# Kernel optimization log

Hardware: AMD Instinct MI355X
Metric: run time of the kernel (lower is better)

## Reference

```python
import jax, jax.numpy as jnp
import numpy as np

E, B, S, H = 8, 16, 512, 1024
LN_EPS = 1e-12


def setup_inputs() -> dict:
    key = jax.random.key(0)
    k = jax.random.split(key, 5)
    return {
        "hidden_states": jax.random.normal(k[0], (B, S, H), dtype=jnp.float32),
        "input_tensor": jax.random.normal(k[1], (B, S, H), dtype=jnp.float32),
        "expert_idx": jax.random.randint(k[2], (B,), 0, E, dtype=jnp.int64)
        if jax.config.jax_enable_x64 else jax.random.randint(k[2], (B,), 0, E, dtype=jnp.int32),
        "W": jax.random.normal(k[3], (E, H, H), dtype=jnp.float32) * (1.0 / np.sqrt(H)),
        "b": jax.random.normal(k[4], (E, H), dtype=jnp.float32) * 0.02,
        "gamma": jnp.ones((H,), dtype=jnp.float32),
        "beta": jnp.zeros((H,), dtype=jnp.float32),
    }


def reference(hidden_states, input_tensor, expert_idx, W, b, gamma, beta):
    # All-expert dense forward, matching single_select_fwd's stacked compute.
    # all_out: [E, B, S, H]
    all_out = jnp.einsum("bsh,ehd->ebsd", hidden_states, W) + b[:, None, None, :]
    # slice_for_expert: pick (expert_idx[b], b) for each batch row -> [B, S, H]
    selected = all_out[expert_idx, jnp.arange(hidden_states.shape[0])]
    # dropout is identity in eval mode; residual + LayerNorm
    x = selected + input_tensor
    mu = jnp.mean(x, axis=-1, keepdims=True)
    var = jnp.mean(jnp.square(x - mu), axis=-1, keepdims=True)
    return (x - mu) * jax.lax.rsqrt(var + LN_EPS) * gamma + beta
```

## Files before the change

kernel.cpp:

```cpp
#include <hip/hip_runtime.h>
#include <hip/hip_bf16.h>

#define BB 16
#define SS 512
#define HH 1024

typedef __attribute__((ext_vector_type(4))) float f32x4;
typedef __attribute__((ext_vector_type(8))) short bhalf8;

static __device__ __forceinline__ unsigned int pack2(float a, float b) {
    __hip_bfloat162 h = __float22bfloat162_rn(make_float2(a, b));
    union { __hip_bfloat162 h; unsigned int u; } cv;
    cv.h = h;
    return cv.u;
}

static __device__ __forceinline__ unsigned short bf16u(float f) {
    union { float f; unsigned int u; } c; c.f = f;
    unsigned int r = c.u + 0x7FFFu + ((c.u >> 16) & 1u);
    return (unsigned short)(r >> 16);
}

static __device__ __forceinline__ float ubf16(unsigned short u) {
    union { unsigned int u; float f; } c; c.u = ((unsigned int)u) << 16;
    return c.f;
}

__global__ __launch_bounds__(256)
void prep_kernel(const float* __restrict__ W, const float* __restrict__ hid,
                 const int* __restrict__ eidx, unsigned short* __restrict__ Wt,
                 unsigned short* __restrict__ hidb)
{
    int bid = blockIdx.x;
    int t = threadIdx.x;
    if (bid < 2048) {
        __shared__ float lds[32 * 132];
        int e  = bid >> 8;
        bool used = false;
        for (int b = 0; b < BB; ++b) used = used || (eidx[b] == e);
        if (!used) return;
        int rem = bid & 255;
        int kt = rem >> 3, dt = rem & 7;
#pragma unroll
        for (int i = 0; i < 4; ++i) {
            int idx = t + i * 256;
            int row = idx >> 5, col4 = idx & 31;
            float4 v = *(const float4*)(W + ((size_t)e << 20)
                        + (size_t)(kt * 32 + row) * HH + dt * 128 + col4 * 4);
            float* dst = &lds[row * 132 + col4 * 4];
            dst[0] = v.x; dst[1] = v.y; dst[2] = v.z; dst[3] = v.w;
        }
        __syncthreads();
        int d = t >> 1, kh = t & 1;
        unsigned int u[8];
#pragma unroll
        for (int p = 0; p < 8; ++p) {
            float a = lds[(kh * 16 + p * 2)     * 132 + d];
            float b = lds[(kh * 16 + p * 2 + 1) * 132 + d];
            u[p] = pack2(a, b);
        }
        unsigned short* dst = Wt + ((size_t)e << 20)
                            + (size_t)(dt * 128 + d) * HH + kt * 32 + kh * 16;
        *reinterpret_cast<uint4*>(dst)     = make_uint4(u[0], u[1], u[2], u[3]);
        *reinterpret_cast<uint4*>(dst + 8) = make_uint4(u[4], u[5], u[6], u[7]);
    } else {
        int bid2 = bid - 2048;
        int r = bid2 * 2 + (t >> 7);
        int col = (t & 127) * 8;
        const float* src = hid + (size_t)r * HH + col;
        float4 v0 = *(const float4*)(src);
        float4 v1 = *(const float4*)(src + 4);
        uint4 o;
        o.x = pack2(v0.x, v0.y); o.y = pack2(v0.z, v0.w);
        o.z = pack2(v1.x, v1.y); o.w = pack2(v1.z, v1.w);
        *reinterpret_cast<uint4*>(hidb + (size_t)r * HH + col) = o;
    }
}

__global__ __launch_bounds__(512, 4)
void gemm8_kernel(const unsigned short* __restrict__ hidb,
                  const int* __restrict__ eidx,
                  const unsigned short* __restrict__ Wt,
                  unsigned short* __restrict__ ybuf)
{
    __shared__ char ldsA[4 * 8192];
    __shared__ char ldsW[4 * 8192];

    int bx  = blockIdx.x;
    int swz = (bx & 7) * 64 + (bx >> 3);
    int bt   = swz >> 5;
    int tile = swz & 31;
    int mt = tile >> 3, nt = tile & 7;
    int e = eidx[bt];

    int t = threadIdx.x, wave = t >> 6, lane = t & 63;
    int l15 = lane & 15, g = lane >> 4;
    int wm = wave >> 1, wn = wave & 1;

    int brow = bt * SS + mt * 128;
    int ncol0 = nt * 128;

    const unsigned short* asrc;
    const unsigned short* wsrc;
    int coff;
    {
        int c = t;
        int line = c >> 3, p = c & 7, q = p ^ (line & 7);
        int row = line * 2 + (q >> 2), s = q & 3;
        asrc = hidb + (size_t)(brow + row) * HH + s * 8;
        wsrc = Wt + ((size_t)e << 20) + (size_t)(ncol0 + row) * HH + s * 8;
        coff = c * 16;
    }

    auto stage = [&](int ks, int b) {
        __builtin_amdgcn_global_load_lds(
            (const __attribute__((address_space(1))) void*)(asrc + ks * 32),
            (__attribute__((address_space(3))) void*)(ldsA + b * 8192 + coff),
            16, 0, 0);
        __builtin_amdgcn_global_load_lds(
            (const __attribute__((address_space(1))) void*)(wsrc + ks * 32),
            (__attribute__((address_space(3))) void*)(ldsW + b * 8192 + coff),
            16, 0, 0);
    };

    f32x4 acc[2][4] = {};

    auto body = [&](int ks, bool do_stage) {
        const char* Af = ldsA + (ks & 3) * 8192;
        const char* Wf = ldsW + (ks & 3) * 8192;
        bhalf8 af[2], bf[4];
#pragma unroll
        for (int mf = 0; mf < 2; ++mf) {
            int r = wm * 32 + mf * 16 + l15;
            int line = r >> 1;
            int p = (g + ((r & 1) << 2)) ^ (line & 7);
            af[mf] = *reinterpret_cast<const bhalf8*>(Af + line * 128 + p * 16);
        }
#pragma unroll
        for (int nf = 0; nf < 4; ++nf) {
            int d = wn * 64 + nf * 16 + l15;
            int line = d >> 1;
            int p = (g + ((d & 1) << 2)) ^ (line & 7);
            bf[nf] = *reinterpret_cast<const bhalf8*>(Wf + line * 128 + p * 16);
        }
        if (do_stage) stage(ks + 3, (ks + 3) & 3);
        __builtin_amdgcn_s_barrier();
        __builtin_amdgcn_s_setprio(1);
#pragma unroll
        for (int mf = 0; mf < 2; ++mf)
#pragma unroll
            for (int nf = 0; nf < 4; ++nf)
                acc[mf][nf] = __builtin_amdgcn_mfma_f32_16x16x32_bf16(
                    af[mf], bf[nf], acc[mf][nf], 0, 0, 0);
        __builtin_amdgcn_s_setprio(0);
    };

    stage(0, 0); stage(1, 1); stage(2, 2);
    asm volatile("s_waitcnt vmcnt(4)" ::: "memory");
    __builtin_amdgcn_s_barrier();

    for (int ks = 0; ks < 29; ++ks) {
        body(ks, true);
        asm volatile("s_waitcnt vmcnt(4)" ::: "memory");
        __builtin_amdgcn_s_barrier();
    }
    body(29, false);
    asm volatile("s_waitcnt vmcnt(2)" ::: "memory");
    __builtin_amdgcn_s_barrier();
    body(30, false);
    asm volatile("s_waitcnt vmcnt(0)" ::: "memory");
    __builtin_amdgcn_s_barrier();
    body(31, false);

#pragma unroll
    for (int nf = 0; nf < 4; ++nf) {
        int dcol = ncol0 + wn * 64 + nf * 16 + l15;
#pragma unroll
        for (int mf = 0; mf < 2; ++mf)
#pragma unroll
            for (int j = 0; j < 4; ++j) {
                int srow = brow + wm * 32 + mf * 16 + g * 4 + j;
                ybuf[(size_t)srow * HH + dcol] = bf16u(acc[mf][nf][j]);
            }
    }
}

__global__ __launch_bounds__(256)
void post_kernel(const unsigned short* __restrict__ ybuf,
                 const float* __restrict__ inp,
                 const int* __restrict__ eidx, const float* __restrict__ bias,
                 const float* __restrict__ gamma, const float* __restrict__ beta,
                 float* __restrict__ out)
{
    int bid = blockIdx.x;
    int row = ((bid & 7) << 10) | (bid >> 3);
    int bt = row >> 9;
    int e = eidx[bt];
    int t = threadIdx.x;

    size_t base = (size_t)row * HH + t * 4;
    ushort4 yv = *reinterpret_cast<const ushort4*>(&ybuf[base]);
    float4 iv = *reinterpret_cast<const float4*>(&inp[base]);
    float4 bv = *reinterpret_cast<const float4*>(&bias[e * HH + t * 4]);
    float4 x;
    x.x = ubf16(yv.x) + iv.x + bv.x;
    x.y = ubf16(yv.y) + iv.y + bv.y;
    x.z = ubf16(yv.z) + iv.z + bv.z;
    x.w = ubf16(yv.w) + iv.w + bv.w;

    float s1 = x.x + x.y + x.z + x.w;
    float s2 = x.x * x.x + x.y * x.y + x.z * x.z + x.w * x.w;
#pragma unroll
    for (int off = 32; off > 0; off >>= 1) {
        s1 += __shfl_xor(s1, off, 64);
        s2 += __shfl_xor(s2, off, 64);
    }
    __shared__ float red[8];
    if ((t & 63) == 0) { red[(t >> 6) * 2] = s1; red[(t >> 6) * 2 + 1] = s2; }
    __syncthreads();
    float S1 = red[0] + red[2] + red[4] + red[6];
    float S2 = red[1] + red[3] + red[5] + red[7];
    float mu  = S1 * (1.0f / HH);
    float var = S2 * (1.0f / HH) - mu * mu;
    float rs = rsqrtf(var + 1e-12f);

    float4 gv = *reinterpret_cast<const float4*>(&gamma[t * 4]);
    float4 be = *reinterpret_cast<const float4*>(&beta[t * 4]);
    float4 o;
    o.x = (x.x - mu) * rs * gv.x + be.x;
    o.y = (x.y - mu) * rs * gv.y + be.y;
    o.z = (x.z - mu) * rs * gv.z + be.z;
    o.w = (x.w - mu) * rs * gv.w + be.w;
    *reinterpret_cast<float4*>(&out[base]) = o;
}

extern "C" void kernel_launch(void* const* d_in, const int* in_sizes, int n_in,
                              void* d_out, int out_size, void* d_ws, size_t ws_size,
                              hipStream_t stream) {
    const float* hid   = (const float*)d_in[0];
    const float* inp   = (const float*)d_in[1];
    const int*   eidx  = (const int*)d_in[2];
    const float* W     = (const float*)d_in[3];
    const float* bias  = (const float*)d_in[4];
    const float* gamma = (const float*)d_in[5];
    const float* beta  = (const float*)d_in[6];
    float* out = (float*)d_out;

    unsigned short* Wt   = (unsigned short*)d_ws;
    unsigned short* hidb = (unsigned short*)((char*)d_ws + (16u << 20));
    unsigned short* ybuf = (unsigned short*)((char*)d_ws + (32u << 20));

    prep_kernel<<<6144, 256, 0, stream>>>(W, hid, eidx, Wt, hidb);
    gemm8_kernel<<<512, 512, 0, stream>>>(hidb, eidx, Wt, ybuf);
    post_kernel<<<BB * SS, 256, 0, stream>>>(ybuf, inp, eidx, bias, gamma, beta, out);
}
```

Baseline: 56.24 us.

## Load W fragments directly from global into registers using k-tiled layout

The prep kernel now writes the transposed bf16 weights in a k-tile-major layout (32-wide k slabs, contiguous per tile). The GEMM kernel drops the LDS staging buffer for W and instead has each lane load its MFMA B fragments straight from global memory into registers, double-buffered one k-step ahead, with adjusted vmcnt waits. This halves LDS usage and removes LDS traffic for W, which may raise occupancy. The cost is uncoalesced-ish per-lane global loads and the W reuse across the two wm waves going through cache instead of LDS.

```diff
diff --git a/kernel.cpp b/kernel.cpp
--- a/kernel.cpp
+++ b/kernel.cpp
@@ -28,7 +28,7 @@
 
 __global__ __launch_bounds__(256)
 void prep_kernel(const float* __restrict__ W, const float* __restrict__ hid,
-                 const int* __restrict__ eidx, unsigned short* __restrict__ Wt,
+                 const int* __restrict__ eidx, unsigned short* __restrict__ Wt2,
                  unsigned short* __restrict__ hidb)
 {
     int bid = blockIdx.x;
@@ -59,8 +59,8 @@
             float b = lds[(kh * 16 + p * 2 + 1) * 132 + d];
             u[p] = pack2(a, b);
         }
-        unsigned short* dst = Wt + ((size_t)e << 20)
-                            + (size_t)(dt * 128 + d) * HH + kt * 32 + kh * 16;
+        unsigned short* dst = Wt2 + ((size_t)e << 20)
+                            + (size_t)kt * 32768 + (size_t)(dt * 128 + d) * 32 + kh * 16;
         *reinterpret_cast<uint4*>(dst)     = make_uint4(u[0], u[1], u[2], u[3]);
         *reinterpret_cast<uint4*>(dst + 8) = make_uint4(u[4], u[5], u[6], u[7]);
     } else {
@@ -80,11 +80,10 @@
 __global__ __launch_bounds__(512, 4)
 void gemm8_kernel(const unsigned short* __restrict__ hidb,
                   const int* __restrict__ eidx,
-                  const unsigned short* __restrict__ Wt,
+                  const unsigned short* __restrict__ Wt2,
                   unsigned short* __restrict__ ybuf)
 {
     __shared__ char ldsA[4 * 8192];
-    __shared__ char ldsW[4 * 8192];
 
     int bx  = blockIdx.x;
     int swz = (bx & 7) * 64 + (bx >> 3);
@@ -101,34 +100,43 @@
     int ncol0 = nt * 128;
 
     const unsigned short* asrc;
-    const unsigned short* wsrc;
     int coff;
     {
         int c = t;
         int line = c >> 3, p = c & 7, q = p ^ (line & 7);
         int row = line * 2 + (q >> 2), s = q & 3;
         asrc = hidb + (size_t)(brow + row) * HH + s * 8;
-        wsrc = Wt + ((size_t)e << 20) + (size_t)(ncol0 + row) * HH + s * 8;
         coff = c * 16;
     }
 
-    auto stage = [&](int ks, int b) {
+    auto stageA = [&](int ks, int b) {
         __builtin_amdgcn_global_load_lds(
             (const __attribute__((address_space(1))) void*)(asrc + ks * 32),
             (__attribute__((address_space(3))) void*)(ldsA + b * 8192 + coff),
             16, 0, 0);
-        __builtin_amdgcn_global_load_lds(
-            (const __attribute__((address_space(1))) void*)(wsrc + ks * 32),
-            (__attribute__((address_space(3))) void*)(ldsW + b * 8192 + coff),
-            16, 0, 0);
     };
 
+    const unsigned short* wlane = Wt2 + ((size_t)e << 20)
+                                + (size_t)(ncol0 + wn * 64 + l15) * 32 + g * 8;
+
+    bhalf8 bf[4], bfp[4];
+    auto loadW = [&](int ks, bhalf8* dst) {
+        const unsigned short* p = wlane + (size_t)ks * 32768;
+#pragma unroll
+        for (int nf = 0; nf < 4; ++nf)
+            dst[nf] = *reinterpret_cast<const bhalf8*>(p + nf * 512);
+    };
+
     f32x4 acc[2][4] = {};
 
-    auto body = [&](int ks, bool do_stage) {
+    stageA(0, 0); stageA(1, 1); stageA(2, 2);
+    loadW(0, bf);
+    asm volatile("s_waitcnt vmcnt(6)" ::: "memory");
+    __builtin_amdgcn_s_barrier();
+
+    for (int ks = 0; ks < 32; ++ks) {
         const char* Af = ldsA + (ks & 3) * 8192;
-        const char* Wf = ldsW + (ks & 3) * 8192;
-        bhalf8 af[2], bf[4];
+        bhalf8 af[2];
 #pragma unroll
         for (int mf = 0; mf < 2; ++mf) {
             int r = wm * 32 + mf * 16 + l15;
@@ -136,14 +144,8 @@
             int p = (g + ((r & 1) << 2)) ^ (line & 7);
             af[mf] = *reinterpret_cast<const bhalf8*>(Af + line * 128 + p * 16);
         }
-#pragma unroll
-        for (int nf = 0; nf < 4; ++nf) {
-            int d = wn * 64 + nf * 16 + l15;
-            int line = d >> 1;
-            int p = (g + ((d & 1) << 2)) ^ (line & 7);
-            bf[nf] = *reinterpret_cast<const bhalf8*>(Wf + line * 128 + p * 16);
-        }
-        if (do_stage) stage(ks + 3, (ks + 3) & 3);
+        if (ks <= 30) loadW(ks + 1, bfp);
+        if (ks <= 28) stageA(ks + 3, (ks + 3) & 3);
         __builtin_amdgcn_s_barrier();
         __builtin_amdgcn_s_setprio(1);
 #pragma unroll
@@ -153,24 +155,13 @@
                 acc[mf][nf] = __builtin_amdgcn_mfma_f32_16x16x32_bf16(
                     af[mf], bf[nf], acc[mf][nf], 0, 0, 0);
         __builtin_amdgcn_s_setprio(0);
-    };
-
-    stage(0, 0); stage(1, 1); stage(2, 2);
-    asm volatile("s_waitcnt vmcnt(4)" ::: "memory");
-    __builtin_amdgcn_s_barrier();
-
-    for (int ks = 0; ks < 29; ++ks) {
-        body(ks, true);
-        asm volatile("s_waitcnt vmcnt(4)" ::: "memory");
+#pragma unroll
+        for (int nf = 0; nf < 4; ++nf) bf[nf] = bfp[nf];
+        if (ks < 29)       { asm volatile("s_waitcnt vmcnt(6)" ::: "memory"); }
+        else if (ks == 29) { asm volatile("s_waitcnt vmcnt(5)" ::: "memory"); }
+        else if (ks == 30) { asm volatile("s_waitcnt vmcnt(4)" ::: "memory"); }
         __builtin_amdgcn_s_barrier();
     }
-    body(29, false);
-    asm volatile("s_waitcnt vmcnt(2)" ::: "memory");
-    __builtin_amdgcn_s_barrier();
-    body(30, false);
-    asm volatile("s_waitcnt vmcnt(0)" ::: "memory");
-    __builtin_amdgcn_s_barrier();
-    body(31, false);
 
 #pragma unroll
     for (int nf = 0; nf < 4; ++nf) {
@@ -246,11 +237,11 @@
     const float* beta  = (const float*)d_in[6];
     float* out = (float*)d_out;
 
-    unsigned short* Wt   = (unsigned short*)d_ws;
+    unsigned short* Wt2  = (unsigned short*)d_ws;
     unsigned short* hidb = (unsigned short*)((char*)d_ws + (16u << 20));
     unsigned short* ybuf = (unsigned short*)((char*)d_ws + (32u << 20));
 
-    prep_kernel<<<6144, 256, 0, stream>>>(W, hid, eidx, Wt, hidb);
-    gemm8_kernel<<<512, 512, 0, stream>>>(hidb, eidx, Wt, ybuf);
+    prep_kernel<<<6144, 256, 0, stream>>>(W, hid, eidx, Wt2, hidb);
+    gemm8_kernel<<<512, 512, 0, stream>>>(hidb, eidx, Wt2, ybuf);
     post_kernel<<<BB * SS, 256, 0, stream>>>(ybuf, inp, eidx, bias, gamma, beta, out);
 }
```

New measurement: 70.92 us. +26.1%, slower.

## Shrink GEMM tile to 128x64 with 4 waves and double buffering

Applied to the files above, without the earlier changes.

Changes the expert GEMM from 128x128 tiles run by 512 threads with a 4-stage LDS ring to 128x64 tiles run by 256 threads with a 2-stage double buffer, launching 1024 blocks instead of 512. Each wave now computes a 64x32 sub-tile, and the hand-tuned vmcnt/barrier schedule is replaced by a __syncthreads at the end of each k-step. The intent is to raise occupancy and block count with a smaller LDS footprint. The cost is shallower prefetch depth, a full memory wait every iteration, and less operand reuse per tile, since the hidden-state tile is now loaded twice as often.

```diff
diff --git a/kernel.cpp b/kernel.cpp
--- a/kernel.cpp
+++ b/kernel.cpp
@@ -77,20 +77,20 @@
     }
 }
 
-__global__ __launch_bounds__(512, 4)
+__global__ __launch_bounds__(256, 5)
 void gemm8_kernel(const unsigned short* __restrict__ hidb,
                   const int* __restrict__ eidx,
                   const unsigned short* __restrict__ Wt,
                   unsigned short* __restrict__ ybuf)
 {
-    __shared__ char ldsA[4 * 8192];
-    __shared__ char ldsW[4 * 8192];
+    __shared__ char ldsA[2 * 8192];
+    __shared__ char ldsW[2 * 4096];
 
     int bx  = blockIdx.x;
-    int swz = (bx & 7) * 64 + (bx >> 3);
-    int bt   = swz >> 5;
-    int tile = swz & 31;
-    int mt = tile >> 3, nt = tile & 7;
+    int swz = (bx & 7) * 128 + (bx >> 3);
+    int bt   = swz >> 6;
+    int rem  = swz & 63;
+    int mt = rem >> 4, nt = rem & 15;
     int e = eidx[bt];
 
     int t = threadIdx.x, wave = t >> 6, lane = t & 63;
@@ -98,88 +98,86 @@
     int wm = wave >> 1, wn = wave & 1;
 
     int brow = bt * SS + mt * 128;
-    int ncol0 = nt * 128;
-
-    const unsigned short* asrc;
+    int ncol0 = nt * 64;
+
+    const unsigned short* asrc[2];
+    int aoff[2];
+#pragma unroll
+    for (int i = 0; i < 2; ++i) {
+        int c = t + i * 256;
+        int line = c >> 3, p = c & 7, q = p ^ (line & 7);
+        int row = line * 2 + (q >> 2), s = q & 3;
+        asrc[i] = hidb + (size_t)(brow + row) * HH + s * 8;
+        aoff[i] = c * 16;
+    }
     const unsigned short* wsrc;
-    int coff;
+    int woff;
     {
         int c = t;
         int line = c >> 3, p = c & 7, q = p ^ (line & 7);
         int row = line * 2 + (q >> 2), s = q & 3;
-        asrc = hidb + (size_t)(brow + row) * HH + s * 8;
         wsrc = Wt + ((size_t)e << 20) + (size_t)(ncol0 + row) * HH + s * 8;
-        coff = c * 16;
-    }
-
-    auto stage = [&](int ks, int b) {
-        __builtin_amdgcn_global_load_lds(
-            (const __attribute__((address_space(1))) void*)(asrc + ks * 32),
-            (__attribute__((address_space(3))) void*)(ldsA + b * 8192 + coff),
-            16, 0, 0);
+        woff = c * 16;
+    }
+
+    auto stage = [&](int ks, int sel) {
+#pragma unroll
+        for (int i = 0; i < 2; ++i)
+            __builtin_amdgcn_global_load_lds(
+                (const __attribute__((address_space(1))) void*)(asrc[i] + ks * 32),
+                (__attribute__((address_space(3))) void*)(ldsA + sel * 8192 + aoff[i]),
+                16, 0, 0);
         __builtin_amdgcn_global_load_lds(
             (const __attribute__((address_space(1))) void*)(wsrc + ks * 32),
-            (__attribute__((address_space(3))) void*)(ldsW + b * 8192 + coff),
+            (__attribute__((address_space(3))) void*)(ldsW + sel * 4096 + woff),
             16, 0, 0);
     };
 
-    f32x4 acc[2][4] = {};
-
-    auto body = [&](int ks, bool do_stage) {
-        const char* Af = ldsA + (ks & 3) * 8192;
-        const char* Wf = ldsW + (ks & 3) * 8192;
-        bhalf8 af[2], bf[4];
-#pragma unroll
-        for (int mf = 0; mf < 2; ++mf) {
-            int r = wm * 32 + mf * 16 + l15;
+    f32x4 acc[4][2] = {};
+
+    stage(0, 0);
+    __syncthreads();
+
+    for (int ks = 0; ks < 32; ++ks) {
+        int sel = ks & 1;
+        if (ks < 31) stage(ks + 1, sel ^ 1);
+
+        const char* Af = ldsA + sel * 8192;
+        const char* Wf = ldsW + sel * 4096;
+        bhalf8 af[4], bf[2];
+#pragma unroll
+        for (int mf = 0; mf < 4; ++mf) {
+            int r = wm * 64 + mf * 16 + l15;
             int line = r >> 1;
             int p = (g + ((r & 1) << 2)) ^ (line & 7);
             af[mf] = *reinterpret_cast<const bhalf8*>(Af + line * 128 + p * 16);
         }
 #pragma unroll
-        for (int nf = 0; nf < 4; ++nf) {
-            int d = wn * 64 + nf * 16 + l15;
+        for (int nf = 0; nf < 2; ++nf) {
+            int d = wn * 32 + nf * 16 + l15;
             int line = d >> 1;
             int p = (g + ((d & 1) << 2)) ^ (line & 7);
             bf[nf] = *reinterpret_cast<const bhalf8*>(Wf + line * 128 + p * 16);
         }
-        if (do_stage) stage(ks + 3, (ks + 3) & 3);
-        __builtin_amdgcn_s_barrier();
         __builtin_amdgcn_s_setprio(1);
 #pragma unroll
-        for (int mf = 0; mf < 2; ++mf)
-#pragma unroll
-            for (int nf = 0; nf < 4; ++nf)
+        for (int mf = 0; mf < 4; ++mf)
+#pragma unroll
+            for (int nf = 0; nf < 2; ++nf)
                 acc[mf][nf] = __builtin_amdgcn_mfma_f32_16x16x32_bf16(
                     af[mf], bf[nf], acc[mf][nf], 0, 0, 0);
         __builtin_amdgcn_s_setprio(0);
-    };
-
-    stage(0, 0); stage(1, 1); stage(2, 2);
-    asm volatile("s_waitcnt vmcnt(4)" ::: "memory");
-    __builtin_amdgcn_s_barrier();
-
-    for (int ks = 0; ks < 29; ++ks) {
-        body(ks, true);
-        asm volatile("s_waitcnt vmcnt(4)" ::: "memory");
-        __builtin_amdgcn_s_barrier();
-    }
-    body(29, false);
-    asm volatile("s_waitcnt vmcnt(2)" ::: "memory");
-    __builtin_amdgcn_s_barrier();
-    body(30, false);
-    asm volatile("s_waitcnt vmcnt(0)" ::: "memory");
-    __builtin_amdgcn_s_barrier();
-    body(31, false);
-
-#pragma unroll
-    for (int nf = 0; nf < 4; ++nf) {
-        int dcol = ncol0 + wn * 64 + nf * 16 + l15;
-#pragma unroll
-        for (int mf = 0; mf < 2; ++mf)
+        __syncthreads();
+    }
+
+#pragma unroll
+    for (int nf = 0; nf < 2; ++nf) {
+        int dcol = ncol0 + wn * 32 + nf * 16 + l15;
+#pragma unroll
+        for (int mf = 0; mf < 4; ++mf)
 #pragma unroll
             for (int j = 0; j < 4; ++j) {
-                int srow = brow + wm * 32 + mf * 16 + g * 4 + j;
+                int srow = brow + wm * 64 + mf * 16 + g * 4 + j;
                 ybuf[(size_t)srow * HH + dcol] = bf16u(acc[mf][nf][j]);
             }
     }
@@ -251,6 +249,6 @@
     unsigned short* ybuf = (unsigned short*)((char*)d_ws + (32u << 20));
 
     prep_kernel<<<6144, 256, 0, stream>>>(W, hid, eidx, Wt, hidb);
-    gemm8_kernel<<<512, 512, 0, stream>>>(hidb, eidx, Wt, ybuf);
+    gemm8_kernel<<<1024, 256, 0, stream>>>(hidb, eidx, Wt, ybuf);
     post_kernel<<<BB * SS, 256, 0, stream>>>(ybuf, inp, eidx, bias, gamma, beta, out);
 }
```

Result: slower. 63.02 us (+12.1%).
